# Optimization experiments

Measured on AMD Instinct MI355X. Metric: run time of the kernel, lower is better.

The kernel has to match this reference:

```python
import jax, jax.numpy as jnp
import numpy as np

N = 12000      # total nodes
T = 6000       # tail (query) nodes
H = 4000       # head (key/value) nodes
D = 256        # att_hidd_dim
NUM_HEADS = 8
HEAD_DIM = D // NUM_HEADS
EDGE_VOCAB = 64


def setup_inputs() -> dict:
    key = jax.random.key(0)
    ks = jax.random.split(key, 16)
    inp = {
        "query": jax.random.normal(ks[0], (N, D), jnp.float32),
        "key": jax.random.normal(ks[1], (N, D), jnp.float32),
        "value": jax.random.normal(ks[2], (N, D), jnp.float32),
        "adj_matrix": jax.random.randint(ks[3], (T, H), 0, 2, jnp.int32),
        "c_indices": jax.random.randint(ks[4], (T, H), 0, EDGE_VOCAB, jnp.int32),
        "ground_ind_tail": jnp.arange(T, dtype=jnp.int32),
        "ground_ind_head": jnp.arange(H, dtype=jnp.int32) + T,  # disjoint bipartite sets
        "Wq": 0.02 * jax.random.normal(ks[5], (D, D), jnp.float32),
        "bq": jnp.zeros((D,), jnp.float32),
        "Wk": 0.02 * jax.random.normal(ks[6], (D, D), jnp.float32),
        "bk": jnp.zeros((D,), jnp.float32),
        "Wv": 0.02 * jax.random.normal(ks[7], (D, D), jnp.float32),
        "bv": jnp.zeros((D,), jnp.float32),
        "Wo": 0.02 * jax.random.normal(ks[8], (D, D), jnp.float32),
        "bo": jnp.zeros((D,), jnp.float32),
        "edge_emb": 0.02 * jax.random.normal(ks[9], (EDGE_VOCAB, NUM_HEADS), jnp.float32),
    }
    return inp


def reference(query, key, value, adj_matrix, c_indices, ground_ind_tail,
              ground_ind_head, Wq, bq, Wk, bk, Wv, bv, Wo, bo, edge_emb):
    scaling = HEAD_DIM ** -0.5
    # gather + project; [heads, T, hd] / [heads, H, hd]
    q_tail = ((query[ground_ind_tail] @ Wq.T + bq) * scaling).reshape(T, NUM_HEADS, HEAD_DIM).swapaxes(0, 1)
    k_head = (key[ground_ind_head] @ Wk.T + bk).reshape(H, NUM_HEADS, HEAD_DIM).swapaxes(0, 1)
    v_head = (value[ground_ind_head] @ Wv.T + bv).reshape(H, NUM_HEADS, HEAD_DIM).swapaxes(0, 1)

    tail_mask = jnp.where(adj_matrix == 0, -1e9, 0.0)[None]              # [1, T, H]
    edge_bias = edge_emb[c_indices].transpose(2, 0, 1)                    # [heads, T, H]

    scores = jnp.einsum('htd,hsd->hts', q_tail, k_head) + tail_mask + edge_bias
    attn = jax.nn.softmax(scores, axis=-1)
    out_tail = jnp.einsum('hts,hsd->htd', attn, v_head)                   # [heads, T, hd]

    attn_all = jnp.zeros((NUM_HEADS, N, HEAD_DIM), query.dtype)
    attn_all = attn_all.at[:, ground_ind_tail].set(out_tail)
    attn_all = attn_all.at[:, ground_ind_head].set(
        query[ground_ind_head].reshape(H, NUM_HEADS, HEAD_DIM).swapaxes(0, 1))
    attn_all = attn_all.swapaxes(0, 1).reshape(N, D)                      # [N, D]
    return attn_all @ Wo.T + bo
```

## Files before the change

### kernel.cpp

```cpp
#include <hip/hip_runtime.h>
#include <hip/hip_bf16.h>

#define T_N 6000
#define H_N 4000
#define N_N 12000
#define DIM 256
#define NHEAD 8
#define HDIM 32
#define SCALING 0.17677669529663687f
#define LOG2E 1.4426950408889634f
#define NTT 375
#define NST 125
#define PCW (NTT * NST * 128)

typedef __attribute__((ext_vector_type(8))) short bf16x8;
typedef __attribute__((ext_vector_type(4))) float f32x4;

union BF8U { bf16x8 v; unsigned int w[4]; __hip_bfloat16 h[8]; unsigned short us[8]; };

static __device__ __forceinline__ unsigned int cvt_pk_bf16(float a, float b) {
  unsigned int r;
  asm("v_cvt_pk_bf16_f32 %0, %1, %2" : "=v"(r) : "v"(a), "v"(b));
  return r;
}

__global__ __launch_bounds__(256) void pack_pc(
    const int* __restrict__ adj, const int* __restrict__ cind,
    unsigned int* __restrict__ pc)
{
  const int stride = gridDim.x * 256;
  for (int i = blockIdx.x * 256 + threadIdx.x; i < PCW; i += stride) {
    const int tl = i & 15;
    const int gi = (i >> 4) & 7;
    const int rem = i >> 7;
    const int st = rem % NST;
    const int tt = rem / NST;
    const int t = tt * 16 + tl;
    const int s0 = st * 32 + gi * 4;
    const int4 c4 = *reinterpret_cast<const int4*>(cind + (size_t)t * H_N + s0);
    const int4 a4 = *reinterpret_cast<const int4*>(adj + (size_t)t * H_N + s0);
    unsigned int w = 0;
    w |= (unsigned)((c4.x & 63) | (a4.x ? 64 : 0));
    w |= (unsigned)((c4.y & 63) | (a4.y ? 64 : 0)) << 8;
    w |= (unsigned)((c4.z & 63) | (a4.z ? 64 : 0)) << 16;
    w |= (unsigned)((c4.w & 63) | (a4.w ? 64 : 0)) << 24;
    pc[i] = w;
  }
}

static __device__ __forceinline__ void proj_body(
    int role, const float* __restrict__ X, const int* __restrict__ idx,
    const float* __restrict__ W, const float* __restrict__ bvec,
    __hip_bfloat16* __restrict__ outf, int rows, float scale, int bx,
    char* As, char* Bs)
{
  const int tid = threadIdx.x;
  const int w = tid >> 6;
  const int lane = tid & 63;
  const int q = lane >> 4;
  const int t = lane & 15;
  const int n0 = (bx & 7) * 32;
  const int m0 = (bx >> 3) * 64;

  for (int i = tid; i < 2048; i += 256) {
    const int row = i >> 5, c16 = i & 31;
    BF8U u;
    u.w[0] = 0; u.w[1] = 0; u.w[2] = 0; u.w[3] = 0;
    const int gr = m0 + row;
    if (gr < rows) {
      const int src = idx ? idx[gr] : gr;
      const float* sp = X + (size_t)src * DIM + c16 * 8;
      const float4 x0 = *reinterpret_cast<const float4*>(sp);
      const float4 x1 = *reinterpret_cast<const float4*>(sp + 4);
      u.w[0] = cvt_pk_bf16(x0.x, x0.y);
      u.w[1] = cvt_pk_bf16(x0.z, x0.w);
      u.w[2] = cvt_pk_bf16(x1.x, x1.y);
      u.w[3] = cvt_pk_bf16(x1.z, x1.w);
    }
    *reinterpret_cast<bf16x8*>(As + ((row * 512 + c16 * 16) ^ ((row & 7) << 4))) = u.v;
  }
  for (int i = tid; i < 1024; i += 256) {
    const int row = i >> 5, c16 = i & 31;
    const float* sp = W + (size_t)(n0 + row) * DIM + c16 * 8;
    const float4 x0 = *reinterpret_cast<const float4*>(sp);
    const float4 x1 = *reinterpret_cast<const float4*>(sp + 4);
    BF8U u;
    u.w[0] = cvt_pk_bf16(x0.x, x0.y);
    u.w[1] = cvt_pk_bf16(x0.z, x0.w);
    u.w[2] = cvt_pk_bf16(x1.x, x1.y);
    u.w[3] = cvt_pk_bf16(x1.z, x1.w);
    *reinterpret_cast<bf16x8*>(Bs + ((row * 512 + c16 * 16) ^ ((row & 7) << 4))) = u.v;
  }
  __syncthreads();

  f32x4 acc0 = {0.f, 0.f, 0.f, 0.f};
  f32x4 acc1 = {0.f, 0.f, 0.f, 0.f};
#pragma unroll
  for (int kk = 0; kk < 8; kk++) {
    const int arow = w * 16 + t;
    const bf16x8 af = *reinterpret_cast<const bf16x8*>(
        As + ((arow * 512 + (kk * 32 + q * 8) * 2) ^ ((arow & 7) << 4)));
    const bf16x8 bf0 = *reinterpret_cast<const bf16x8*>(
        Bs + ((t * 512 + (kk * 32 + q * 8) * 2) ^ ((t & 7) << 4)));
    const bf16x8 bf1 = *reinterpret_cast<const bf16x8*>(
        Bs + (((16 + t) * 512 + (kk * 32 + q * 8) * 2) ^ (((16 + t) & 7) << 4)));
    acc0 = __builtin_amdgcn_mfma_f32_16x16x32_bf16(af, bf0, acc0, 0, 0, 0);
    acc1 = __builtin_amdgcn_mfma_f32_16x16x32_bf16(af, bf1, acc1, 0, 0, 0);
  }

#pragma unroll
  for (int r = 0; r < 4; r++) {
    const int grow = m0 + w * 16 + q * 4 + r;
    if (grow >= rows) continue;
    const float a0 = acc0[r], a1 = acc1[r];
    const int jj[2] = {n0 + t, n0 + 16 + t};
    const float vv[2] = {(a0 + bvec[jj[0]]) * scale, (a1 + bvec[jj[1]]) * scale};
#pragma unroll
    for (int f = 0; f < 2; f++) {
      const int j = jj[f];
      const __hip_bfloat16 hv = __float2bfloat16(vv[f]);
      const int h = j >> 5;
      size_t idxo;
      if (role == 1) {
        idxo = (((size_t)h * NTT + (grow >> 4)) * 64 + ((j & 31) >> 3) * 16 +
                (grow & 15)) * 8 + (j & 7);
      } else if (role == 2) {
        idxo = (((size_t)h * 250 + (grow >> 4)) * 64 + ((j & 31) >> 3) * 16 +
                (grow & 15)) * 8 + (j & 7);
      } else {
        const int dh = (j & 31) >> 4, dl = j & 15;
        const int sl = grow & 31;
        const int qv = (sl & 15) >> 2;
        const int ev = (sl & 3) | (((sl >> 4) & 1) << 2);
        idxo = ((((size_t)h * 2 + dh) * NST + (grow >> 5)) * 64 +
                qv * 16 + dl) * 8 + ev;
      }
      outf[idxo] = hv;
    }
  }
}

#define NBQ 752
#define NBK 504
#define NBV 504
#define NBC 1000

__global__ __launch_bounds__(256) void proj_all(
    const float* __restrict__ query, const float* __restrict__ key,
    const float* __restrict__ value, const int* __restrict__ tail_idx,
    const int* __restrict__ head_idx,
    const float* __restrict__ Wq, const float* __restrict__ bq,
    const float* __restrict__ Wk, const float* __restrict__ bk,
    const float* __restrict__ Wv, const float* __restrict__ bv,
    __hip_bfloat16* __restrict__ Qf, __hip_bfloat16* __restrict__ Kf,
    __hip_bfloat16* __restrict__ Vf, __hip_bfloat16* __restrict__ Ab)
{
  __shared__ __align__(16) char As[64 * 512];
  __shared__ __align__(16) char Bs[32 * 512];

  const int bx = blockIdx.x;
  if (bx < NBQ) {
    proj_body(1, query, tail_idx, Wq, bq, Qf, T_N, SCALING * LOG2E, bx, As, Bs);
  } else if (bx < NBQ + NBK) {
    proj_body(2, key, head_idx, Wk, bk, Kf, H_N, 1.f, bx - NBQ, As, Bs);
  } else if (bx < NBQ + NBK + NBV) {
    proj_body(3, value, head_idx, Wv, bv, Vf, H_N, 1.f, bx - NBQ - NBK, As, Bs);
  } else {
    const int b = bx - NBQ - NBK - NBV;
    const int rr = b * 4 + (threadIdx.x >> 6);
    const int lane = threadIdx.x & 63;
    const int row = head_idx[rr];
    const float4 v = *reinterpret_cast<const float4*>(
        query + (size_t)row * DIM + lane * 4);
    uint2 o;
    o.x = cvt_pk_bf16(v.x, v.y);
    o.y = cvt_pk_bf16(v.z, v.w);
    *reinterpret_cast<uint2*>(Ab + (size_t)row * DIM + lane * 4) = o;
  }
}

__global__ __launch_bounds__(256, 8) void attn_mfma(
    const __hip_bfloat16* __restrict__ Qf, const __hip_bfloat16* __restrict__ Kf,
    const __hip_bfloat16* __restrict__ Vf, const unsigned int* __restrict__ pc,
    const float* __restrict__ edge_emb, const int* __restrict__ tail_idx,
    __hip_bfloat16* __restrict__ Ab)
{
  __shared__ float tab[128];
  __shared__ float mg[3][64][10];

  const int tid = threadIdx.x;
  const int cs = tid >> 6;
  const int lane = tid & 63;
  const int q = lane >> 4;
  const int t = lane & 15;
  const int h = blockIdx.y;
  const int tt = blockIdx.x;
  const int hbase = h * HDIM;

  if (tid < 128) {
    tab[tid] = (tid < 64) ? -1e9f : edge_emb[(tid - 64) * NHEAD + h] * LOG2E;
  }

  const bf16x8 qf = *reinterpret_cast<const bf16x8*>(
      Qf + (((size_t)h * NTT + tt) * 64 + lane) * 8);

  const int stBeg = (cs * NST) >> 2;
  const int stEnd = ((cs + 1) * NST) >> 2;

  const unsigned int* pcp = pc + (size_t)(tt * NST + stBeg) * 128 + q * 16 + t;
  const __hip_bfloat16* kp = Kf + (((size_t)h * 250 + stBeg * 2) * 64 + lane) * 8;
  const __hip_bfloat16* vp = Vf + (((size_t)h * 2 * NST + stBeg) * 64 + lane) * 8;
  const size_t VD = (size_t)NST * 64 * 8;

  f32x4 oacc0 = {0.f, 0.f, 0.f, 0.f};
  f32x4 oacc1 = {0.f, 0.f, 0.f, 0.f};
  f32x4 lacc  = {0.f, 0.f, 0.f, 0.f};

  BF8U ones;
#pragma unroll
  for (int e = 0; e < 8; e++) ones.us[e] = 0x3F80;

  unsigned int npc0 = pcp[0], npc1 = pcp[64];
  bf16x8 nk0 = *reinterpret_cast<const bf16x8*>(kp);
  bf16x8 nk1 = *reinterpret_cast<const bf16x8*>(kp + 512);
  bf16x8 nv0 = *reinterpret_cast<const bf16x8*>(vp);
  bf16x8 nv1 = *reinterpret_cast<const bf16x8*>(vp + VD);

  __syncthreads();

  for (int st = stBeg; st < stEnd; ++st) {
    const unsigned int cpc0 = npc0, cpc1 = npc1;
    const bf16x8 kf0 = nk0, kf1 = nk1, vf0 = nv0, vf1 = nv1;

    const f32x4 z = {0.f, 0.f, 0.f, 0.f};
    const f32x4 s_lo = __builtin_amdgcn_mfma_f32_16x16x32_bf16(kf0, qf, z, 0, 0, 0);
    const f32x4 s_hi = __builtin_amdgcn_mfma_f32_16x16x32_bf16(kf1, qf, z, 0, 0, 0);

    if (st + 1 < stEnd) {
      pcp += 128; kp += 1024; vp += 512;
      npc0 = pcp[0];
      npc1 = pcp[64];
      nk0 = *reinterpret_cast<const bf16x8*>(kp);
      nk1 = *reinterpret_cast<const bf16x8*>(kp + 512);
      nv0 = *reinterpret_cast<const bf16x8*>(vp);
      nv1 = *reinterpret_cast<const bf16x8*>(vp + VD);
    }

    float p[8];
#pragma unroll
    for (int r = 0; r < 4; r++) {
      const float bb0 = tab[(cpc0 >> (r * 8)) & 127u];
      const float bb1 = tab[(cpc1 >> (r * 8)) & 127u];
      p[r] = __builtin_amdgcn_exp2f(s_lo[r] + bb0);
      p[r + 4] = __builtin_amdgcn_exp2f(s_hi[r] + bb1);
    }

    BF8U pu;
    pu.w[0] = cvt_pk_bf16(p[0], p[1]);
    pu.w[1] = cvt_pk_bf16(p[2], p[3]);
    pu.w[2] = cvt_pk_bf16(p[4], p[5]);
    pu.w[3] = cvt_pk_bf16(p[6], p[7]);

    oacc0 = __builtin_amdgcn_mfma_f32_16x16x32_bf16(vf0, pu.v, oacc0, 0, 0, 0);
    oacc1 = __builtin_amdgcn_mfma_f32_16x16x32_bf16(vf1, pu.v, oacc1, 0, 0, 0);
    lacc  = __builtin_amdgcn_mfma_f32_16x16x32_bf16(ones.v, pu.v, lacc, 0, 0, 0);
  }

  const float Lc = lacc[0];

  if (cs) {
#pragma unroll
    for (int r = 0; r < 4; r++) {
      mg[cs - 1][lane][r] = oacc0[r];
      mg[cs - 1][lane][4 + r] = oacc1[r];
    }
    mg[cs - 1][lane][8] = Lc;
  }
  __syncthreads();
  if (!cs) {
    float L = Lc;
    float o[8];
#pragma unroll
    for (int r = 0; r < 8; r++) o[r] = (r < 4) ? oacc0[r] : oacc1[r - 4];
#pragma unroll
    for (int c = 0; c < 3; c++) {
      L += mg[c][lane][8];
#pragma unroll
      for (int r = 0; r < 8; r++) o[r] += mg[c][lane][r];
    }
    const float inv = 1.f / L;
    const int row = tail_idx[tt * 16 + t];
    __hip_bfloat16* dst = Ab + (size_t)row * DIM + hbase + q * 4;
    uint2 w0, w1;
    w0.x = cvt_pk_bf16(o[0] * inv, o[1] * inv);
    w0.y = cvt_pk_bf16(o[2] * inv, o[3] * inv);
    w1.x = cvt_pk_bf16(o[4] * inv, o[5] * inv);
    w1.y = cvt_pk_bf16(o[6] * inv, o[7] * inv);
    *reinterpret_cast<uint2*>(dst) = w0;
    *reinterpret_cast<uint2*>(dst + 16) = w1;
  }
}

__global__ __launch_bounds__(256) void oproj_mfma(
    const __hip_bfloat16* __restrict__ Ab, const float* __restrict__ Wo,
    const float* __restrict__ bo, float* __restrict__ out)
{
  __shared__ __align__(16) char As[64 * 512];
  __shared__ __align__(16) char Bs[32 * 512];

  const int tid = threadIdx.x;
  const int w = tid >> 6;
  const int lane = tid & 63;
  const int bl = lane & 15;
  const int q = lane >> 4;
  const int n0 = blockIdx.x * 32;
  const int m0 = blockIdx.y * 64;

  for (int i = tid; i < 2048; i += 256) {
    const int row = i >> 5, c16 = i & 31;
    bf16x8 v = {0, 0, 0, 0, 0, 0, 0, 0};
    const int gr = m0 + row;
    if (gr < N_N)
      v = *reinterpret_cast<const bf16x8*>(Ab + (size_t)gr * DIM + c16 * 8);
    *reinterpret_cast<bf16x8*>(As + ((row * 512 + c16 * 16) ^ ((row & 7) << 4))) = v;
  }
  for (int i = tid; i < 1024; i += 256) {
    const int row = i >> 5, c16 = i & 31;
    const float* src = Wo + (size_t)(n0 + row) * DIM + c16 * 8;
    const float4 x0 = *reinterpret_cast<const float4*>(src);
    const float4 x1 = *reinterpret_cast<const float4*>(src + 4);
    BF8U u;
    u.w[0] = cvt_pk_bf16(x0.x, x0.y);
    u.w[1] = cvt_pk_bf16(x0.z, x0.w);
    u.w[2] = cvt_pk_bf16(x1.x, x1.y);
    u.w[3] = cvt_pk_bf16(x1.z, x1.w);
    *reinterpret_cast<bf16x8*>(Bs + ((row * 512 + c16 * 16) ^ ((row & 7) << 4))) = u.v;
  }
  __syncthreads();

  f32x4 acc0 = {0.f, 0.f, 0.f, 0.f};
  f32x4 acc1 = {0.f, 0.f, 0.f, 0.f};
#pragma unroll
  for (int kk = 0; kk < 8; kk++) {
    const int arow = w * 16 + bl;
    const bf16x8 af = *reinterpret_cast<const bf16x8*>(
        As + ((arow * 512 + (kk * 32 + q * 8) * 2) ^ ((arow & 7) << 4)));
    const bf16x8 bf0 = *reinterpret_cast<const bf16x8*>(
        Bs + ((bl * 512 + (kk * 32 + q * 8) * 2) ^ ((bl & 7) << 4)));
    const int brow = 16 + bl;
    const bf16x8 bf1 = *reinterpret_cast<const bf16x8*>(
        Bs + ((brow * 512 + (kk * 32 + q * 8) * 2) ^ ((brow & 7) << 4)));
    acc0 = __builtin_amdgcn_mfma_f32_16x16x32_bf16(af, bf0, acc0, 0, 0, 0);
    acc1 = __builtin_amdgcn_mfma_f32_16x16x32_bf16(af, bf1, acc1, 0, 0, 0);
  }

#pragma unroll
  for (int r = 0; r < 4; r++) {
    const int grow = m0 + w * 16 + q * 4 + r;
    if (grow < N_N) {
      const int j0 = n0 + bl;
      const int j1 = n0 + 16 + bl;
      out[(size_t)grow * DIM + j0] = acc0[r] + bo[j0];
      out[(size_t)grow * DIM + j1] = acc1[r] + bo[j1];
    }
  }
}

extern "C" void kernel_launch(void* const* d_in, const int* in_sizes, int n_in,
                              void* d_out, int out_size, void* d_ws, size_t ws_size,
                              hipStream_t stream)
{
  const float* query    = (const float*)d_in[0];
  const float* key      = (const float*)d_in[1];
  const float* value    = (const float*)d_in[2];
  const int*   adj      = (const int*)d_in[3];
  const int*   cind     = (const int*)d_in[4];
  const int*   tail_idx = (const int*)d_in[5];
  const int*   head_idx = (const int*)d_in[6];
  const float* Wq = (const float*)d_in[7];
  const float* bq = (const float*)d_in[8];
  const float* Wk = (const float*)d_in[9];
  const float* bk = (const float*)d_in[10];
  const float* Wv = (const float*)d_in[11];
  const float* bv = (const float*)d_in[12];
  const float* Wo = (const float*)d_in[13];
  const float* bo = (const float*)d_in[14];
  const float* edge_emb = (const float*)d_in[15];

  float* out = (float*)d_out;
  char*  ws  = (char*)d_ws;

  __hip_bfloat16* Ab = (__hip_bfloat16*)ws;
  __hip_bfloat16* Qf = (__hip_bfloat16*)(ws + 6144000);
  __hip_bfloat16* Kf = (__hip_bfloat16*)(ws + 9216000);
  __hip_bfloat16* Vf = (__hip_bfloat16*)(ws + 11264000);
  unsigned int*   pc = (unsigned int*)(ws + 13312000);

  hipMemsetAsync(Ab + (size_t)10000 * DIM, 0,
                 (size_t)2000 * DIM * sizeof(__hip_bfloat16), stream);

  pack_pc<<<dim3(2048), dim3(256), 0, stream>>>(adj, cind, pc);

  proj_all<<<dim3(NBQ + NBK + NBV + NBC), dim3(256), 0, stream>>>(
      query, key, value, tail_idx, head_idx,
      Wq, bq, Wk, bk, Wv, bv, Qf, Kf, Vf, Ab);

  attn_mfma<<<dim3(NTT, NHEAD), dim3(256), 0, stream>>>(
      Qf, Kf, Vf, pc, edge_emb, tail_idx, Ab);

  oproj_mfma<<<dim3(8, (N_N + 63) / 64), dim3(256), 0, stream>>>(
      Ab, Wo, bo, out);
}
```

Measured before the change: 158.0 us.

## Process two query tiles per attention block to reuse K/V fragments

Each attention block now handles two 16-row tail tiles against the same K/V fragments, halving K/V global loads per query row. The packed adjacency/edge buffer is re-laid out so both tiles' words are contiguous, and pack_pc is rewritten to stage words through swizzled LDS for coalesced stores. The grid is reordered with heads on x, and s_setprio is added around the MFMA groups. The extra accumulators raise register use, which is why launch bounds drop to 4 waves, and V is no longer prefetched a step ahead.

```diff
diff --git a/kernel.cpp b/kernel.cpp
--- a/kernel.cpp
+++ b/kernel.cpp
@@ -10,8 +10,8 @@
 #define SCALING 0.17677669529663687f
 #define LOG2E 1.4426950408889634f
 #define NTT 375
+#define NTP 188
 #define NST 125
-#define PCW (NTT * NST * 128)
 
 typedef __attribute__((ext_vector_type(8))) short bf16x8;
 typedef __attribute__((ext_vector_type(4))) float f32x4;
@@ -24,18 +24,26 @@
   return r;
 }
 
+static __device__ __forceinline__ int swz256(int w) {
+  return w ^ (((w >> 5) & 3) << 3);
+}
+
 __global__ __launch_bounds__(256) void pack_pc(
     const int* __restrict__ adj, const int* __restrict__ cind,
     unsigned int* __restrict__ pc)
 {
-  const int stride = gridDim.x * 256;
-  for (int i = blockIdx.x * 256 + threadIdx.x; i < PCW; i += stride) {
-    const int tl = i & 15;
-    const int gi = (i >> 4) & 7;
-    const int rem = i >> 7;
-    const int st = rem % NST;
-    const int tt = rem / NST;
-    const int t = tt * 16 + tl;
+  __shared__ unsigned int lds[256];
+  const int bid = blockIdx.x;
+  const int tid = threadIdx.x;
+  const int ttp = bid / 125;
+  const int st  = bid % 125;
+  const int tb  = tid >> 7;
+  const int tl  = (tid >> 3) & 15;
+  const int gi  = tid & 7;
+  const int tt  = ttp * 2 + tb;
+
+  if (tt < NTT) {
+    const int t  = tt * 16 + tl;
     const int s0 = st * 32 + gi * 4;
     const int4 c4 = *reinterpret_cast<const int4*>(cind + (size_t)t * H_N + s0);
     const int4 a4 = *reinterpret_cast<const int4*>(adj + (size_t)t * H_N + s0);
@@ -44,8 +52,16 @@
     w |= (unsigned)((c4.y & 63) | (a4.y ? 64 : 0)) << 8;
     w |= (unsigned)((c4.z & 63) | (a4.z ? 64 : 0)) << 16;
     w |= (unsigned)((c4.w & 63) | (a4.w ? 64 : 0)) << 24;
-    pc[i] = w;
-  }
+    const int wloc = tb * 128 + gi * 16 + tl;
+    lds[swz256(wloc)] = w;
+  }
+  __syncthreads();
+
+  const bool full = (ttp < 187);
+  const size_t base = full ? (size_t)bid * 256
+                           : (size_t)5984000 + (size_t)st * 128;
+  const int nw = full ? 256 : 128;
+  if (tid < nw) pc[base + tid] = lds[swz256(tid)];
 }
 
 static __device__ __forceinline__ void proj_body(
@@ -179,125 +195,173 @@
   }
 }
 
-__global__ __launch_bounds__(256, 8) void attn_mfma(
+__global__ __launch_bounds__(256, 4) void attn_mfma(
     const __hip_bfloat16* __restrict__ Qf, const __hip_bfloat16* __restrict__ Kf,
     const __hip_bfloat16* __restrict__ Vf, const unsigned int* __restrict__ pc,
     const float* __restrict__ edge_emb, const int* __restrict__ tail_idx,
     __hip_bfloat16* __restrict__ Ab)
 {
   __shared__ float tab[128];
-  __shared__ float mg[3][64][10];
+  __shared__ float mg[3][64][18];
 
   const int tid = threadIdx.x;
   const int cs = tid >> 6;
   const int lane = tid & 63;
   const int q = lane >> 4;
   const int t = lane & 15;
-  const int h = blockIdx.y;
-  const int tt = blockIdx.x;
+  const int h = blockIdx.x;
+  const int ttp = blockIdx.y;
   const int hbase = h * HDIM;
 
   if (tid < 128) {
     tab[tid] = (tid < 64) ? -1e9f : edge_emb[(tid - 64) * NHEAD + h] * LOG2E;
   }
 
-  const bf16x8 qf = *reinterpret_cast<const bf16x8*>(
-      Qf + (((size_t)h * NTT + tt) * 64 + lane) * 8);
+  const bool full = (ttp < 187);
+  const int tAt = ttp * 2;
+  const int tBt = full ? (ttp * 2 + 1) : 374;
+
+  const bf16x8 qfA = *reinterpret_cast<const bf16x8*>(
+      Qf + (((size_t)h * NTT + tAt) * 64 + lane) * 8);
+  const bf16x8 qfB = *reinterpret_cast<const bf16x8*>(
+      Qf + (((size_t)h * NTT + tBt) * 64 + lane) * 8);
 
   const int stBeg = (cs * NST) >> 2;
   const int stEnd = ((cs + 1) * NST) >> 2;
 
-  const unsigned int* pcp = pc + (size_t)(tt * NST + stBeg) * 128 + q * 16 + t;
+  const size_t pbase = full ? ((size_t)(ttp * 125 + stBeg) * 256)
+                            : ((size_t)5984000 + (size_t)stBeg * 128);
+  const int pcStep = full ? 256 : 128;
+  const int pbOff  = full ? 128 : 0;
+  const unsigned int* pcp = pc + pbase + q * 16 + t;
   const __hip_bfloat16* kp = Kf + (((size_t)h * 250 + stBeg * 2) * 64 + lane) * 8;
   const __hip_bfloat16* vp = Vf + (((size_t)h * 2 * NST + stBeg) * 64 + lane) * 8;
   const size_t VD = (size_t)NST * 64 * 8;
 
-  f32x4 oacc0 = {0.f, 0.f, 0.f, 0.f};
-  f32x4 oacc1 = {0.f, 0.f, 0.f, 0.f};
-  f32x4 lacc  = {0.f, 0.f, 0.f, 0.f};
+  f32x4 oaccA0 = {0.f, 0.f, 0.f, 0.f};
+  f32x4 oaccA1 = {0.f, 0.f, 0.f, 0.f};
+  f32x4 oaccB0 = {0.f, 0.f, 0.f, 0.f};
+  f32x4 oaccB1 = {0.f, 0.f, 0.f, 0.f};
+  f32x4 laccA  = {0.f, 0.f, 0.f, 0.f};
+  f32x4 laccB  = {0.f, 0.f, 0.f, 0.f};
 
   BF8U ones;
 #pragma unroll
   for (int e = 0; e < 8; e++) ones.us[e] = 0x3F80;
 
-  unsigned int npc0 = pcp[0], npc1 = pcp[64];
+  unsigned int npcA0 = pcp[0], npcA1 = pcp[64];
+  unsigned int npcB0 = pcp[pbOff], npcB1 = pcp[pbOff + 64];
   bf16x8 nk0 = *reinterpret_cast<const bf16x8*>(kp);
   bf16x8 nk1 = *reinterpret_cast<const bf16x8*>(kp + 512);
-  bf16x8 nv0 = *reinterpret_cast<const bf16x8*>(vp);
-  bf16x8 nv1 = *reinterpret_cast<const bf16x8*>(vp + VD);
 
   __syncthreads();
 
   for (int st = stBeg; st < stEnd; ++st) {
-    const unsigned int cpc0 = npc0, cpc1 = npc1;
-    const bf16x8 kf0 = nk0, kf1 = nk1, vf0 = nv0, vf1 = nv1;
+    const unsigned int cA0 = npcA0, cA1 = npcA1, cB0 = npcB0, cB1 = npcB1;
+    const bf16x8 kf0 = nk0, kf1 = nk1;
+
+    const bf16x8 vf0 = *reinterpret_cast<const bf16x8*>(vp);
+    const bf16x8 vf1 = *reinterpret_cast<const bf16x8*>(vp + VD);
+    vp += 512;
 
     const f32x4 z = {0.f, 0.f, 0.f, 0.f};
-    const f32x4 s_lo = __builtin_amdgcn_mfma_f32_16x16x32_bf16(kf0, qf, z, 0, 0, 0);
-    const f32x4 s_hi = __builtin_amdgcn_mfma_f32_16x16x32_bf16(kf1, qf, z, 0, 0, 0);
+    __builtin_amdgcn_s_setprio(1);
+    const f32x4 sA_lo = __builtin_amdgcn_mfma_f32_16x16x32_bf16(kf0, qfA, z, 0, 0, 0);
+    const f32x4 sA_hi = __builtin_amdgcn_mfma_f32_16x16x32_bf16(kf1, qfA, z, 0, 0, 0);
+    const f32x4 sB_lo = __builtin_amdgcn_mfma_f32_16x16x32_bf16(kf0, qfB, z, 0, 0, 0);
+    const f32x4 sB_hi = __builtin_amdgcn_mfma_f32_16x16x32_bf16(kf1, qfB, z, 0, 0, 0);
+    __builtin_amdgcn_s_setprio(0);
 
     if (st + 1 < stEnd) {
-      pcp += 128; kp += 1024; vp += 512;
-      npc0 = pcp[0];
-      npc1 = pcp[64];
+      pcp += pcStep; kp += 1024;
+      npcA0 = pcp[0];
+      npcA1 = pcp[64];
+      npcB0 = pcp[pbOff];
+      npcB1 = pcp[pbOff + 64];
       nk0 = *reinterpret_cast<const bf16x8*>(kp);
       nk1 = *reinterpret_cast<const bf16x8*>(kp + 512);
-      nv0 = *reinterpret_cast<const bf16x8*>(vp);
-      nv1 = *reinterpret_cast<const bf16x8*>(vp + VD);
-    }
-
-    float p[8];
+    }
+
+    float pA[8], pB[8];
 #pragma unroll
     for (int r = 0; r < 4; r++) {
-      const float bb0 = tab[(cpc0 >> (r * 8)) & 127u];
-      const float bb1 = tab[(cpc1 >> (r * 8)) & 127u];
-      p[r] = __builtin_amdgcn_exp2f(s_lo[r] + bb0);
-      p[r + 4] = __builtin_amdgcn_exp2f(s_hi[r] + bb1);
-    }
-
-    BF8U pu;
-    pu.w[0] = cvt_pk_bf16(p[0], p[1]);
-    pu.w[1] = cvt_pk_bf16(p[2], p[3]);
-    pu.w[2] = cvt_pk_bf16(p[4], p[5]);
-    pu.w[3] = cvt_pk_bf16(p[6], p[7]);
-
-    oacc0 = __builtin_amdgcn_mfma_f32_16x16x32_bf16(vf0, pu.v, oacc0, 0, 0, 0);
-    oacc1 = __builtin_amdgcn_mfma_f32_16x16x32_bf16(vf1, pu.v, oacc1, 0, 0, 0);
-    lacc  = __builtin_amdgcn_mfma_f32_16x16x32_bf16(ones.v, pu.v, lacc, 0, 0, 0);
-  }
-
-  const float Lc = lacc[0];
+      pA[r]     = __builtin_amdgcn_exp2f(sA_lo[r] + tab[(cA0 >> (r * 8)) & 127u]);
+      pA[r + 4] = __builtin_amdgcn_exp2f(sA_hi[r] + tab[(cA1 >> (r * 8)) & 127u]);
+      pB[r]     = __builtin_amdgcn_exp2f(sB_lo[r] + tab[(cB0 >> (r * 8)) & 127u]);
+      pB[r + 4] = __builtin_amdgcn_exp2f(sB_hi[r] + tab[(cB1 >> (r * 8)) & 127u]);
+    }
+
+    BF8U puA, puB;
+    puA.w[0] = cvt_pk_bf16(pA[0], pA[1]);
+    puA.w[1] = cvt_pk_bf16(pA[2], pA[3]);
+    puA.w[2] = cvt_pk_bf16(pA[4], pA[5]);
+    puA.w[3] = cvt_pk_bf16(pA[6], pA[7]);
+    puB.w[0] = cvt_pk_bf16(pB[0], pB[1]);
+    puB.w[1] = cvt_pk_bf16(pB[2], pB[3]);
+    puB.w[2] = cvt_pk_bf16(pB[4], pB[5]);
+    puB.w[3] = cvt_pk_bf16(pB[6], pB[7]);
+
+    __builtin_amdgcn_s_setprio(1);
+    oaccA0 = __builtin_amdgcn_mfma_f32_16x16x32_bf16(vf0, puA.v, oaccA0, 0, 0, 0);
+    oaccA1 = __builtin_amdgcn_mfma_f32_16x16x32_bf16(vf1, puA.v, oaccA1, 0, 0, 0);
+    laccA  = __builtin_amdgcn_mfma_f32_16x16x32_bf16(ones.v, puA.v, laccA, 0, 0, 0);
+    oaccB0 = __builtin_amdgcn_mfma_f32_16x16x32_bf16(vf0, puB.v, oaccB0, 0, 0, 0);
+    oaccB1 = __builtin_amdgcn_mfma_f32_16x16x32_bf16(vf1, puB.v, oaccB1, 0, 0, 0);
+    laccB  = __builtin_amdgcn_mfma_f32_16x16x32_bf16(ones.v, puB.v, laccB, 0, 0, 0);
+    __builtin_amdgcn_s_setprio(0);
+  }
+
+  float LA = laccA[0];
+  float LB = laccB[0];
 
   if (cs) {
 #pragma unroll
     for (int r = 0; r < 4; r++) {
-      mg[cs - 1][lane][r] = oacc0[r];
-      mg[cs - 1][lane][4 + r] = oacc1[r];
-    }
-    mg[cs - 1][lane][8] = Lc;
+      mg[cs - 1][lane][r]      = oaccA0[r];
+      mg[cs - 1][lane][4 + r]  = oaccA1[r];
+      mg[cs - 1][lane][8 + r]  = oaccB0[r];
+      mg[cs - 1][lane][12 + r] = oaccB1[r];
+    }
+    mg[cs - 1][lane][16] = LA;
+    mg[cs - 1][lane][17] = LB;
   }
   __syncthreads();
   if (!cs) {
-    float L = Lc;
-    float o[8];
-#pragma unroll
-    for (int r = 0; r < 8; r++) o[r] = (r < 4) ? oacc0[r] : oacc1[r - 4];
+    float oA[8], oB[8];
+#pragma unroll
+    for (int r = 0; r < 4; r++) {
+      oA[r] = oaccA0[r]; oA[4 + r] = oaccA1[r];
+      oB[r] = oaccB0[r]; oB[4 + r] = oaccB1[r];
+    }
 #pragma unroll
     for (int c = 0; c < 3; c++) {
-      L += mg[c][lane][8];
-#pragma unroll
-      for (int r = 0; r < 8; r++) o[r] += mg[c][lane][r];
-    }
-    const float inv = 1.f / L;
-    const int row = tail_idx[tt * 16 + t];
-    __hip_bfloat16* dst = Ab + (size_t)row * DIM + hbase + q * 4;
-    uint2 w0, w1;
-    w0.x = cvt_pk_bf16(o[0] * inv, o[1] * inv);
-    w0.y = cvt_pk_bf16(o[2] * inv, o[3] * inv);
-    w1.x = cvt_pk_bf16(o[4] * inv, o[5] * inv);
-    w1.y = cvt_pk_bf16(o[6] * inv, o[7] * inv);
-    *reinterpret_cast<uint2*>(dst) = w0;
-    *reinterpret_cast<uint2*>(dst + 16) = w1;
+      LA += mg[c][lane][16];
+      LB += mg[c][lane][17];
+#pragma unroll
+      for (int r = 0; r < 8; r++) {
+        oA[r] += mg[c][lane][r];
+        oB[r] += mg[c][lane][8 + r];
+      }
+    }
+    const float invA = 1.f / LA;
+    const float invB = 1.f / LB;
+    const int rowA = tail_idx[tAt * 16 + t];
+    const int rowB = tail_idx[tBt * 16 + t];
+    __hip_bfloat16* dstA = Ab + (size_t)rowA * DIM + hbase + q * 4;
+    __hip_bfloat16* dstB = Ab + (size_t)rowB * DIM + hbase + q * 4;
+    uint2 wa0, wa1, wb0, wb1;
+    wa0.x = cvt_pk_bf16(oA[0] * invA, oA[1] * invA);
+    wa0.y = cvt_pk_bf16(oA[2] * invA, oA[3] * invA);
+    wa1.x = cvt_pk_bf16(oA[4] * invA, oA[5] * invA);
+    wa1.y = cvt_pk_bf16(oA[6] * invA, oA[7] * invA);
+    wb0.x = cvt_pk_bf16(oB[0] * invB, oB[1] * invB);
+    wb0.y = cvt_pk_bf16(oB[2] * invB, oB[3] * invB);
+    wb1.x = cvt_pk_bf16(oB[4] * invB, oB[5] * invB);
+    wb1.y = cvt_pk_bf16(oB[6] * invB, oB[7] * invB);
+    *reinterpret_cast<uint2*>(dstA) = wa0;
+    *reinterpret_cast<uint2*>(dstA + 16) = wa1;
+    *reinterpret_cast<uint2*>(dstB) = wb0;
+    *reinterpret_cast<uint2*>(dstB + 16) = wb1;
   }
 }
 
@@ -399,13 +463,13 @@
   hipMemsetAsync(Ab + (size_t)10000 * DIM, 0,
                  (size_t)2000 * DIM * sizeof(__hip_bfloat16), stream);
 
-  pack_pc<<<dim3(2048), dim3(256), 0, stream>>>(adj, cind, pc);
+  pack_pc<<<dim3(NTP * NST), dim3(256), 0, stream>>>(adj, cind, pc);
 
   proj_all<<<dim3(NBQ + NBK + NBV + NBC), dim3(256), 0, stream>>>(
       query, key, value, tail_idx, head_idx,
       Wq, bq, Wk, bk, Wv, bv, Qf, Kf, Vf, Ab);
 
-  attn_mfma<<<dim3(NTT, NHEAD), dim3(256), 0, stream>>>(
+  attn_mfma<<<dim3(NHEAD, NTP), dim3(256), 0, stream>>>(
       Qf, Kf, Vf, pc, edge_emb, tail_idx, Ab);
 
   oproj_mfma<<<dim3(8, (N_N + 63) / 64), dim3(256), 0, stream>>>(
```

Result: faster. 139.2 us (-11.9%).

## Fuse adjacency/edge packing into attention, split keys across blocks with merge kernel

Applied to the files above, without the earlier changes.

Removes the pack_pc pre-pass: the attention kernel now reads adj and c_indices directly as int4 vectors and indexes an 8-head edge-bias table in LDS. Each block handles all 8 heads for a 16-row tail tile (one wave per head) over half the key range. Partial outputs and row sums go to global buffers that a new merge kernel combines and normalises. s_setprio is wrapped around the MFMAs. Reading the raw int32 masks is shared across heads instead of going through a packed intermediate, at the cost of an extra launch and a global round trip for the partials.

```diff
diff --git a/kernel.cpp b/kernel.cpp
--- a/kernel.cpp
+++ b/kernel.cpp
@@ -11,7 +11,6 @@
 #define LOG2E 1.4426950408889634f
 #define NTT 375
 #define NST 125
-#define PCW (NTT * NST * 128)
 
 typedef __attribute__((ext_vector_type(8))) short bf16x8;
 typedef __attribute__((ext_vector_type(4))) float f32x4;
@@ -22,30 +21,6 @@
   unsigned int r;
   asm("v_cvt_pk_bf16_f32 %0, %1, %2" : "=v"(r) : "v"(a), "v"(b));
   return r;
-}
-
-__global__ __launch_bounds__(256) void pack_pc(
-    const int* __restrict__ adj, const int* __restrict__ cind,
-    unsigned int* __restrict__ pc)
-{
-  const int stride = gridDim.x * 256;
-  for (int i = blockIdx.x * 256 + threadIdx.x; i < PCW; i += stride) {
-    const int tl = i & 15;
-    const int gi = (i >> 4) & 7;
-    const int rem = i >> 7;
-    const int st = rem % NST;
-    const int tt = rem / NST;
-    const int t = tt * 16 + tl;
-    const int s0 = st * 32 + gi * 4;
-    const int4 c4 = *reinterpret_cast<const int4*>(cind + (size_t)t * H_N + s0);
-    const int4 a4 = *reinterpret_cast<const int4*>(adj + (size_t)t * H_N + s0);
-    unsigned int w = 0;
-    w |= (unsigned)((c4.x & 63) | (a4.x ? 64 : 0));
-    w |= (unsigned)((c4.y & 63) | (a4.y ? 64 : 0)) << 8;
-    w |= (unsigned)((c4.z & 63) | (a4.z ? 64 : 0)) << 16;
-    w |= (unsigned)((c4.w & 63) | (a4.w ? 64 : 0)) << 24;
-    pc[i] = w;
-  }
 }
 
 static __device__ __forceinline__ void proj_body(
@@ -179,35 +154,38 @@
   }
 }
 
-__global__ __launch_bounds__(256, 8) void attn_mfma(
+__global__ __launch_bounds__(512, 4) void attn_fused(
     const __hip_bfloat16* __restrict__ Qf, const __hip_bfloat16* __restrict__ Kf,
-    const __hip_bfloat16* __restrict__ Vf, const unsigned int* __restrict__ pc,
-    const float* __restrict__ edge_emb, const int* __restrict__ tail_idx,
-    __hip_bfloat16* __restrict__ Ab)
-{
-  __shared__ float tab[128];
-  __shared__ float mg[3][64][10];
+    const __hip_bfloat16* __restrict__ Vf, const int* __restrict__ adj,
+    const int* __restrict__ cind, const float* __restrict__ edge_emb,
+    float* __restrict__ Opart, float* __restrict__ Lpart)
+{
+  __shared__ float tab[NHEAD][128];
 
   const int tid = threadIdx.x;
-  const int cs = tid >> 6;
+  const int h = tid >> 6;
   const int lane = tid & 63;
   const int q = lane >> 4;
   const int t = lane & 15;
-  const int h = blockIdx.y;
-  const int tt = blockIdx.x;
-  const int hbase = h * HDIM;
-
-  if (tid < 128) {
-    tab[tid] = (tid < 64) ? -1e9f : edge_emb[(tid - 64) * NHEAD + h] * LOG2E;
-  }
+  const int bx = blockIdx.x;
+  const int tt = bx >> 1;
+  const int sh = bx & 1;
+  const int t0 = tt * 16;
+
+  for (int i = tid; i < NHEAD * 128; i += 512) {
+    const int hh = i >> 7, ii = i & 127;
+    tab[hh][ii] = (ii < 64) ? -1e9f : edge_emb[(ii - 64) * NHEAD + hh] * LOG2E;
+  }
+
+  const int stBeg = sh ? 63 : 0;
+  const int stEnd = sh ? NST : 63;
+
+  const int* crow = cind + (size_t)(t0 + t) * H_N + q * 4;
+  const int* arow = adj + (size_t)(t0 + t) * H_N + q * 4;
 
   const bf16x8 qf = *reinterpret_cast<const bf16x8*>(
       Qf + (((size_t)h * NTT + tt) * 64 + lane) * 8);
 
-  const int stBeg = (cs * NST) >> 2;
-  const int stEnd = ((cs + 1) * NST) >> 2;
-
-  const unsigned int* pcp = pc + (size_t)(tt * NST + stBeg) * 128 + q * 16 + t;
   const __hip_bfloat16* kp = Kf + (((size_t)h * 250 + stBeg * 2) * 64 + lane) * 8;
   const __hip_bfloat16* vp = Vf + (((size_t)h * 2 * NST + stBeg) * 64 + lane) * 8;
   const size_t VD = (size_t)NST * 64 * 8;
@@ -220,7 +198,10 @@
 #pragma unroll
   for (int e = 0; e < 8; e++) ones.us[e] = 0x3F80;
 
-  unsigned int npc0 = pcp[0], npc1 = pcp[64];
+  int4 ncl = *reinterpret_cast<const int4*>(crow + stBeg * 32);
+  int4 nch = *reinterpret_cast<const int4*>(crow + stBeg * 32 + 16);
+  int4 nal = *reinterpret_cast<const int4*>(arow + stBeg * 32);
+  int4 nah = *reinterpret_cast<const int4*>(arow + stBeg * 32 + 16);
   bf16x8 nk0 = *reinterpret_cast<const bf16x8*>(kp);
   bf16x8 nk1 = *reinterpret_cast<const bf16x8*>(kp + 512);
   bf16x8 nv0 = *reinterpret_cast<const bf16x8*>(vp);
@@ -229,30 +210,37 @@
   __syncthreads();
 
   for (int st = stBeg; st < stEnd; ++st) {
-    const unsigned int cpc0 = npc0, cpc1 = npc1;
+    const int4 cl = ncl, ch = nch, al = nal, ah = nah;
     const bf16x8 kf0 = nk0, kf1 = nk1, vf0 = nv0, vf1 = nv1;
 
     const f32x4 z = {0.f, 0.f, 0.f, 0.f};
+    __builtin_amdgcn_s_setprio(1);
     const f32x4 s_lo = __builtin_amdgcn_mfma_f32_16x16x32_bf16(kf0, qf, z, 0, 0, 0);
     const f32x4 s_hi = __builtin_amdgcn_mfma_f32_16x16x32_bf16(kf1, qf, z, 0, 0, 0);
+    __builtin_amdgcn_s_setprio(0);
 
     if (st + 1 < stEnd) {
-      pcp += 128; kp += 1024; vp += 512;
-      npc0 = pcp[0];
-      npc1 = pcp[64];
+      const int so = (st + 1) * 32;
+      ncl = *reinterpret_cast<const int4*>(crow + so);
+      nch = *reinterpret_cast<const int4*>(crow + so + 16);
+      nal = *reinterpret_cast<const int4*>(arow + so);
+      nah = *reinterpret_cast<const int4*>(arow + so + 16);
+      kp += 1024; vp += 512;
       nk0 = *reinterpret_cast<const bf16x8*>(kp);
       nk1 = *reinterpret_cast<const bf16x8*>(kp + 512);
       nv0 = *reinterpret_cast<const bf16x8*>(vp);
       nv1 = *reinterpret_cast<const bf16x8*>(vp + VD);
     }
 
+    const int cls[4] = {cl.x, cl.y, cl.z, cl.w};
+    const int chs[4] = {ch.x, ch.y, ch.z, ch.w};
+    const int als[4] = {al.x, al.y, al.z, al.w};
+    const int ahs[4] = {ah.x, ah.y, ah.z, ah.w};
     float p[8];
 #pragma unroll
     for (int r = 0; r < 4; r++) {
-      const float bb0 = tab[(cpc0 >> (r * 8)) & 127u];
-      const float bb1 = tab[(cpc1 >> (r * 8)) & 127u];
-      p[r] = __builtin_amdgcn_exp2f(s_lo[r] + bb0);
-      p[r + 4] = __builtin_amdgcn_exp2f(s_hi[r] + bb1);
+      p[r]     = __builtin_amdgcn_exp2f(s_lo[r] + tab[h][cls[r] + (als[r] << 6)]);
+      p[r + 4] = __builtin_amdgcn_exp2f(s_hi[r] + tab[h][chs[r] + (ahs[r] << 6)]);
     }
 
     BF8U pu;
@@ -261,44 +249,49 @@
     pu.w[2] = cvt_pk_bf16(p[4], p[5]);
     pu.w[3] = cvt_pk_bf16(p[6], p[7]);
 
+    __builtin_amdgcn_s_setprio(1);
     oacc0 = __builtin_amdgcn_mfma_f32_16x16x32_bf16(vf0, pu.v, oacc0, 0, 0, 0);
     oacc1 = __builtin_amdgcn_mfma_f32_16x16x32_bf16(vf1, pu.v, oacc1, 0, 0, 0);
     lacc  = __builtin_amdgcn_mfma_f32_16x16x32_bf16(ones.v, pu.v, lacc, 0, 0, 0);
-  }
-
-  const float Lc = lacc[0];
-
-  if (cs) {
-#pragma unroll
-    for (int r = 0; r < 4; r++) {
-      mg[cs - 1][lane][r] = oacc0[r];
-      mg[cs - 1][lane][4 + r] = oacc1[r];
-    }
-    mg[cs - 1][lane][8] = Lc;
-  }
-  __syncthreads();
-  if (!cs) {
-    float L = Lc;
-    float o[8];
-#pragma unroll
-    for (int r = 0; r < 8; r++) o[r] = (r < 4) ? oacc0[r] : oacc1[r - 4];
-#pragma unroll
-    for (int c = 0; c < 3; c++) {
-      L += mg[c][lane][8];
-#pragma unroll
-      for (int r = 0; r < 8; r++) o[r] += mg[c][lane][r];
-    }
-    const float inv = 1.f / L;
-    const int row = tail_idx[tt * 16 + t];
-    __hip_bfloat16* dst = Ab + (size_t)row * DIM + hbase + q * 4;
-    uint2 w0, w1;
-    w0.x = cvt_pk_bf16(o[0] * inv, o[1] * inv);
-    w0.y = cvt_pk_bf16(o[2] * inv, o[3] * inv);
-    w1.x = cvt_pk_bf16(o[4] * inv, o[5] * inv);
-    w1.y = cvt_pk_bf16(o[6] * inv, o[7] * inv);
-    *reinterpret_cast<uint2*>(dst) = w0;
-    *reinterpret_cast<uint2*>(dst + 16) = w1;
-  }
+    __builtin_amdgcn_s_setprio(0);
+  }
+
+  float* op = Opart + ((size_t)bx * NHEAD + h) * 512 + lane * 8;
+  *reinterpret_cast<f32x4*>(op) = oacc0;
+  *reinterpret_cast<f32x4*>(op + 4) = oacc1;
+  if (lane < 16) Lpart[(size_t)bx * 128 + h * 16 + t] = lacc[0];
+}
+
+__global__ __launch_bounds__(512) void merge_out(
+    const float* __restrict__ Opart, const float* __restrict__ Lpart,
+    const int* __restrict__ tail_idx, __hip_bfloat16* __restrict__ Ab)
+{
+  const int tt = blockIdx.x;
+  const int tid = threadIdx.x;
+  const int h = tid >> 6;
+  const int lane = tid & 63;
+  const int q = lane >> 4;
+  const int t = lane & 15;
+
+  const size_t b0 = ((size_t)(tt * 2) * NHEAD + h) * 512 + lane * 8;
+  const size_t b1 = ((size_t)(tt * 2 + 1) * NHEAD + h) * 512 + lane * 8;
+  const f32x4 a0 = *reinterpret_cast<const f32x4*>(Opart + b0);
+  const f32x4 a1 = *reinterpret_cast<const f32x4*>(Opart + b0 + 4);
+  const f32x4 c0 = *reinterpret_cast<const f32x4*>(Opart + b1);
+  const f32x4 c1 = *reinterpret_cast<const f32x4*>(Opart + b1 + 4);
+  const float L = Lpart[(size_t)(tt * 2) * 128 + h * 16 + t] +
+                  Lpart[(size_t)(tt * 2 + 1) * 128 + h * 16 + t];
+  const float inv = 1.f / L;
+
+  const int row = tail_idx[tt * 16 + t];
+  __hip_bfloat16* dst = Ab + (size_t)row * DIM + h * HDIM + q * 4;
+  uint2 w0, w1;
+  w0.x = cvt_pk_bf16((a0[0] + c0[0]) * inv, (a0[1] + c0[1]) * inv);
+  w0.y = cvt_pk_bf16((a0[2] + c0[2]) * inv, (a0[3] + c0[3]) * inv);
+  w1.x = cvt_pk_bf16((a1[0] + c1[0]) * inv, (a1[1] + c1[1]) * inv);
+  w1.y = cvt_pk_bf16((a1[2] + c1[2]) * inv, (a1[3] + c1[3]) * inv);
+  *reinterpret_cast<uint2*>(dst) = w0;
+  *reinterpret_cast<uint2*>(dst + 16) = w1;
 }
 
 __global__ __launch_bounds__(256) void oproj_mfma(
@@ -394,19 +387,20 @@
   __hip_bfloat16* Qf = (__hip_bfloat16*)(ws + 6144000);
   __hip_bfloat16* Kf = (__hip_bfloat16*)(ws + 9216000);
   __hip_bfloat16* Vf = (__hip_bfloat16*)(ws + 11264000);
-  unsigned int*   pc = (unsigned int*)(ws + 13312000);
+  float* Opart = (float*)(ws + 13312000);
+  float* Lpart = (float*)(ws + 25600000);
 
   hipMemsetAsync(Ab + (size_t)10000 * DIM, 0,
                  (size_t)2000 * DIM * sizeof(__hip_bfloat16), stream);
-
-  pack_pc<<<dim3(2048), dim3(256), 0, stream>>>(adj, cind, pc);
 
   proj_all<<<dim3(NBQ + NBK + NBV + NBC), dim3(256), 0, stream>>>(
       query, key, value, tail_idx, head_idx,
       Wq, bq, Wk, bk, Wv, bv, Qf, Kf, Vf, Ab);
 
-  attn_mfma<<<dim3(NTT, NHEAD), dim3(256), 0, stream>>>(
-      Qf, Kf, Vf, pc, edge_emb, tail_idx, Ab);
+  attn_fused<<<dim3(NTT * 2), dim3(512), 0, stream>>>(
+      Qf, Kf, Vf, adj, cind, edge_emb, Opart, Lpart);
+
+  merge_out<<<dim3(NTT), dim3(512), 0, stream>>>(Opart, Lpart, tail_idx, Ab);
 
   oproj_mfma<<<dim3(8, (N_N + 63) / 64), dim3(256), 0, stream>>>(
       Ab, Wo, bo, out);
```

New measurement: 273.6 us. 1.73x slower.
